# Kernel tuning notes

Measured on AMD Instinct MI355X. Metric: run time of the kernel, lower is better.

## Reference

```python
import jax, jax.numpy as jnp
import numpy as np

B, S, W, V, H, L = 128, 128, 16, 128, 512, 64


def setup_inputs() -> dict:
    key = jax.random.key(0)
    ks = jax.random.split(key, 12)
    chars = jax.random.randint(ks[0], (B, S, W), 0, V, dtype=jnp.int32)
    # pack_padded_sequence requires descending lengths; force max length == S for static shapes
    lengths = jnp.sort(jax.random.randint(ks[1], (B,), 1, S + 1, dtype=jnp.int32))[::-1]
    lengths = lengths.at[0].set(S)
    s = 1.0 / np.sqrt(H)
    s2 = 1.0 / np.sqrt(2 * H)

    def u(k, shape, sc):
        return jax.random.uniform(k, shape, jnp.float32, -sc, sc)

    return {
        "chars": chars,
        "lengths": lengths,
        "forget": jnp.float32(0.5),
        "W_ih_f": u(ks[2], (3 * H, V), s),
        "W_hh_f": u(ks[3], (3 * H, H), s),
        "b_ih_f": u(ks[4], (3 * H,), s),
        "b_hh_f": u(ks[5], (3 * H,), s),
        "W_ih_b": u(ks[6], (3 * H, V), s),
        "W_hh_b": u(ks[7], (3 * H, H), s),
        "b_ih_b": u(ks[8], (3 * H,), s),
        "b_hh_b": u(ks[9], (3 * H,), s),
        "W_lin": u(ks[10], (L, 2 * H), s2),
        "b_lin": u(ks[11], (L,), s2),
    }


def _fofe(chars, forget):
    # z = f*z + onehot applied only at nonzero chars => weight f^(# nonzero chars after k)
    mask = (chars != 0).astype(jnp.float32)                              # [B,S,W]
    cnt = jnp.flip(jnp.cumsum(jnp.flip(mask, -1), -1), -1) - mask        # suffix count
    wts = mask * jnp.power(forget, cnt)                                  # [B,S,W]
    oh = jax.nn.one_hot(chars, V, dtype=jnp.float32)                     # [B,S,W,V]
    return jnp.einsum('bsw,bswv->bsv', wts, oh)                          # [B,S,V]


def _gru_dir(x, mask, W_ih, W_hh, b_ih, b_hh):
    # x: [S,B,V], mask: [S,B] (1.0 where t < length). PyTorch GRU cell math.
    xw = jnp.einsum('sbv,gv->sbg', x, W_ih) + b_ih                       # [S,B,3H]
    h0 = jnp.zeros((x.shape[1], H), jnp.float32)

    def step(h, inp):
        xw_t, m = inp
        hw = h @ W_hh.T + b_hh
        xr, xz, xn = jnp.split(xw_t, 3, -1)
        hr, hz, hn = jnp.split(hw, 3, -1)
        r = jax.nn.sigmoid(xr + hr)
        z = jax.nn.sigmoid(xz + hz)
        n = jnp.tanh(xn + r * hn)
        h_new = (1.0 - z) * n + z * h
        m_ = m[:, None]
        h = jnp.where(m_ > 0, h_new, h)
        return h, h_new * m_  # packed-seq semantics: zero output past length

    _, ys = jax.lax.scan(step, h0, (xw, mask))
    return ys  # [S,B,H]


def _forward(chars, lengths, forget, W_ih_f, W_hh_f, b_ih_f, b_hh_f,
             W_ih_b, W_hh_b, b_ih_b, b_hh_b, W_lin, b_lin):
    x = _fofe(chars, forget)                                             # [B,S,V]
    t = jnp.arange(S)
    valid = t[None, :] < lengths[:, None]                                # [B,S]
    mask = valid.astype(jnp.float32).T                                   # [S,B]

    out_f = _gru_dir(x.transpose(1, 0, 2), mask, W_ih_f, W_hh_f, b_ih_f, b_hh_f)

    # backward direction: reverse each sequence within its own length
    idx = jnp.clip(lengths[:, None] - 1 - t[None, :], 0, S - 1)          # [B,S]
    x_rev = jnp.take_along_axis(x, idx[:, :, None], axis=1)              # [B,S,V]
    out_b_rev = _gru_dir(x_rev.transpose(1, 0, 2), mask, W_ih_b, W_hh_b, b_ih_b, b_hh_b)
    out_b = jnp.take_along_axis(out_b_rev.transpose(1, 0, 2), idx[:, :, None], axis=1)
    out_b = out_b * valid[:, :, None].astype(jnp.float32)

    out = jnp.concatenate([out_f.transpose(1, 0, 2), out_b], axis=-1)    # [B,S,2H]
    out = out @ W_lin.T + b_lin                                          # [B,S,L]
    # faithful to torch: out.view(-1, L, S) is a raw reshape, NOT a transpose
    return out.reshape(-1, L, S)


def reference(chars, lengths, forget, W_ih_f, W_hh_f, b_ih_f, b_hh_f,
              W_ih_b, W_hh_b, b_ih_b, b_hh_b, W_lin, b_lin):
    return _forward(chars, lengths, forget, W_ih_f, W_hh_f, b_ih_f, b_hh_f,
                    W_ih_b, W_hh_b, b_ih_b, b_hh_b, W_lin, b_lin)
```

## Files before the change

kernel.cpp:

```cpp
#include <hip/hip_runtime.h>
#include <hip/hip_bf16.h>

#define B_ 128
#define S_ 128
#define W_ 16
#define V_ 128
#define H_ 512
#define L_ 64

typedef _Float16 f16x8 __attribute__((ext_vector_type(8)));
typedef float f32x4 __attribute__((ext_vector_type(4)));

__device__ __forceinline__ float sigm(float v) { return 1.0f / (1.0f + __expf(-v)); }
__device__ __forceinline__ float tanhf_(float v) { return 1.0f - 2.0f / (1.0f + __expf(2.0f * v)); }

__device__ __forceinline__ unsigned short f16bits(_Float16 h) {
    return __builtin_bit_cast(unsigned short, h);
}

#define OFF_SLOT  1048576
#define OFF_FLAG  1064960
#define OFF_XHI   1065024
#define OFF_XLO   5259328
#define OFF_WH    9453632
#define OFF_SMALL 13385792
#define OFF_YCAT  13672832
#define OFF_WLH   47227264
#define OFF_WLL   47358336

__global__ void detect_kernel(const unsigned* __restrict__ w, int* __restrict__ flag) {
    __shared__ int sv[256];
    int tid = threadIdx.x;
    unsigned word = w[tid];
    unsigned e = (word >> 7) & 0xFFu;
    sv[tid] = (e >= 64u && e <= 126u) ? 1 : 0;
    __syncthreads();
    for (int s = 128; s > 0; s >>= 1) {
        if (tid < s) sv[tid] += sv[tid + s];
        __syncthreads();
    }
    if (tid == 0) *flag = (sv[0] >= 160) ? 1 : 0;
}

__global__ void prep_whalf(const void* __restrict__ whhf, const void* __restrict__ whhb,
                           const void* __restrict__ wihf, const void* __restrict__ wihb,
                           _Float16* __restrict__ dst, const int* __restrict__ flag) {
    int i = blockIdx.x * 256 + threadIdx.x;
    const void* src;
    int off;
    if (i < 786432)       { src = whhf; off = i; }
    else if (i < 1572864) { src = whhb; off = i - 786432; }
    else if (i < 1769472) { src = wihf; off = i - 1572864; }
    else                  { src = wihb; off = i - 1769472; }
    float v = (*flag) ? __bfloat162float(((const __hip_bfloat16*)src)[off])
                      : ((const float*)src)[off];
    dst[i] = (_Float16)v;
}

__global__ void prep_small(const void* __restrict__ bihf, const void* __restrict__ bhhf,
                           const void* __restrict__ bihb, const void* __restrict__ bhhb,
                           const void* __restrict__ wlin, const void* __restrict__ blin,
                           const void* __restrict__ fg,
                           float* __restrict__ dst, const int* __restrict__ flag) {
    int i = blockIdx.x * 256 + threadIdx.x;
    if (i >= 71745) return;
    const void* src;
    int off;
    if (i < 1536)       { src = bihf; off = i; }
    else if (i < 3072)  { src = bhhf; off = i - 1536; }
    else if (i < 4608)  { src = bihb; off = i - 3072; }
    else if (i < 6144)  { src = bhhb; off = i - 4608; }
    else if (i < 71680) { src = wlin; off = i - 6144; }
    else if (i < 71744) { src = blin; off = i - 71680; }
    else                { src = fg;   off = 0; }
    float v = (*flag) ? __bfloat162float(((const __hip_bfloat16*)src)[off])
                      : ((const float*)src)[off];
    dst[i] = v;
}

__global__ void prep_wlin(const void* __restrict__ wlin,
                          _Float16* __restrict__ whi, _Float16* __restrict__ wlo,
                          const int* __restrict__ flag) {
    int i = blockIdx.x * 256 + threadIdx.x;
    float v = (*flag) ? __bfloat162float(((const __hip_bfloat16*)wlin)[i])
                      : ((const float*)wlin)[i];
    _Float16 hi = (_Float16)v;
    whi[i] = hi;
    wlo[i] = (_Float16)(v - (float)hi);
}

__global__ void fofe_kernel(const int* __restrict__ chars,
                            const float* __restrict__ fg,
                            unsigned short* __restrict__ xhi,
                            unsigned short* __restrict__ xlo) {
    __shared__ int cS[2][W_];
    int tid = threadIdx.x;
    int sub = tid >> 7;
    int v = tid & 127;
    int bi = blockIdx.x * 2 + sub;
    if (v < W_) cS[sub][v] = chars[bi * W_ + v];
    __syncthreads();
    float f = fg[0];
    float wt[W_];
    float cur = 1.0f;
#pragma unroll
    for (int w = W_ - 1; w >= 0; --w) {
        bool m = (cS[sub][w] != 0);
        wt[w] = m ? cur : 0.0f;
        if (m) cur *= f;
    }
    float acc = 0.0f;
#pragma unroll
    for (int w = 0; w < W_; ++w) acc += (cS[sub][w] == v) ? wt[w] : 0.0f;
    _Float16 hi = (_Float16)acc;
    _Float16 lo = (_Float16)(acc - (float)hi);
    xhi[(size_t)bi * V_ + v] = f16bits(hi);
    xlo[(size_t)bi * V_ + v] = f16bits(lo);
}

__launch_bounds__(256, 1)
__global__ void gru_kernel(const int* __restrict__ lengths,
                           const _Float16* __restrict__ wh,
                           const float* __restrict__ biasF,
                           const unsigned short* __restrict__ xhi,
                           const unsigned short* __restrict__ xlo,
                           unsigned* __restrict__ hbuf,
                           unsigned* __restrict__ slots,
                           _Float16* __restrict__ Ycat) {
    (void)slots;
    constexpr int RSTR = 656;
    __shared__ _Float16 Ahi[16 * RSTR];
    __shared__ _Float16 Alo[16 * RSTR];
    __shared__ int lenS[16];

    const int tid = threadIdx.x;
    const int chain = blockIdx.x & 15;
    const int blk = blockIdx.x >> 4;
    const int d = chain & 1;
    const int bg = chain >> 1;
    const int b0 = bg * 16;
    const int wave = tid >> 6;
    const int lane = tid & 63;
    const int quad = lane >> 4;
    const int col = lane & 15;
    const int j0w = (blk * 4 + wave) * 16;

    const _Float16* Whh = wh + (d ? 786432 : 0);
    const _Float16* Wih = wh + 1572864 + (d ? 196608 : 0);
    const float* bih = biasF + (d ? 3072 : 0);
    const float* bhh = biasF + 1536 + (d ? 3072 : 0);

    if (tid < 16) lenS[tid] = lengths[b0 + tid];
    __syncthreads();

    const int g_r = j0w + col;

    f16x8 br[20], bz[20], bn[20];
#pragma unroll
    for (int kk = 0; kk < 16; ++kk) {
        int k = kk * 32 + quad * 8;
        br[kk] = *(const f16x8*)(Whh + (size_t)(g_r)*H_ + k);
        bz[kk] = *(const f16x8*)(Whh + (size_t)(512 + g_r) * H_ + k);
        bn[kk] = *(const f16x8*)(Whh + (size_t)(1024 + g_r) * H_ + k);
    }
#pragma unroll
    for (int kk = 16; kk < 20; ++kk) {
        int k = (kk - 16) * 32 + quad * 8;
        br[kk] = *(const f16x8*)(Wih + (size_t)(g_r)*V_ + k);
        bz[kk] = *(const f16x8*)(Wih + (size_t)(512 + g_r) * V_ + k);
        bn[kk] = *(const f16x8*)(Wih + (size_t)(1024 + g_r) * V_ + k);
    }

    const float bias_r = bih[g_r] + bhh[g_r];
    const float bias_z = bih[512 + g_r] + bhh[512 + g_r];
    const float bihn = bih[1024 + g_r];
    const float bhhn = bhh[1024 + g_r];

    int len4[4];
#pragma unroll
    for (int i = 0; i < 4; ++i) len4[i] = lenS[quad * 4 + i];
    const int maxlen = lenS[0];

    float h_own[4] = {0.f, 0.f, 0.f, 0.f};

    const _Float16* arh = &Ahi[col * RSTR + quad * 8];
    const _Float16* arl = &Alo[col * RSTR + quad * 8];

    const int xb = tid >> 4;
    const int xv8 = (tid & 15) * 8;

    const unsigned long long tagMsk = (1ULL << 16) | (1ULL << 48);

    for (int t = 0; t < S_; ++t) {
        if (t < maxlen) {
            const int par = t & 1;
            int lxb = lenS[xb];
            int sxb = d ? max(0, lxb - 1 - t) : t;
            int4 xh4 = *(const int4*)(xhi + ((size_t)(b0 + xb) * S_ + sxb) * V_ + xv8);
            int4 xl4 = *(const int4*)(xlo + ((size_t)(b0 + xb) * S_ + sxb) * V_ + xv8);

            unsigned* hrp = hbuf + ((size_t)(par * 2 + d) * B_ + b0) * H_;
            unsigned long long hv[16];
            if (t > 0) {
                const unsigned te = ((((unsigned)(t - 1)) >> 1) & 1u) ^ 1u;
                const unsigned long long tagPat =
                    ((unsigned long long)te << 16) | ((unsigned long long)te << 48);
                unsigned pend = 0xFFFFu;
                unsigned round = 0;
                while (true) {
#pragma unroll
                    for (int i = 0; i < 16; ++i)
                        if (pend & (1u << i))
                            hv[i] = __hip_atomic_load(
                                (const unsigned long long*)(hrp + (size_t)i * H_ + tid * 2),
                                __ATOMIC_RELAXED, __HIP_MEMORY_SCOPE_AGENT);
                    unsigned np = 0;
#pragma unroll
                    for (int i = 0; i < 16; ++i)
                        if ((pend & (1u << i)) && (hv[i] & tagMsk) != tagPat) np |= (1u << i);
                    pend = np;
                    if (!pend) break;
                    ++round;
                    if (round > 4u) __builtin_amdgcn_s_sleep(1);
                    if ((round & 31u) == 31u)
                        __builtin_amdgcn_fence(__ATOMIC_ACQUIRE, "agent");
                    if (round > 400000u) break;
                }
            } else {
#pragma unroll
                for (int i = 0; i < 16; ++i) hv[i] = 0ULL;
            }

            *(int4*)&Ahi[xb * RSTR + 512 + xv8] = xh4;
            *(int4*)&Alo[xb * RSTR + 512 + xv8] = xl4;
#pragma unroll
            for (int i = 0; i < 16; ++i) {
                unsigned p0 = (unsigned)hv[i];
                unsigned p1 = (unsigned)(hv[i] >> 32);
                unsigned hi2 = (p0 & 0xffffu) | (p1 << 16);
                unsigned lo2 = ((p0 >> 16) | (p1 & 0xffff0000u)) & ~0x00010001u;
                *(unsigned*)&Ahi[i * RSTR + tid * 2] = hi2;
                *(unsigned*)&Alo[i * RSTR + tid * 2] = lo2;
            }
            __syncthreads();

            f32x4 accr = {0.f, 0.f, 0.f, 0.f};
            f32x4 accz = {0.f, 0.f, 0.f, 0.f};
            f32x4 acchn = {0.f, 0.f, 0.f, 0.f};
            f32x4 accxn = {0.f, 0.f, 0.f, 0.f};
#pragma unroll
            for (int kk = 0; kk < 16; ++kk) {
                f16x8 ah = *(const f16x8*)(arh + kk * 32);
                f16x8 al = *(const f16x8*)(arl + kk * 32);
                accr = __builtin_amdgcn_mfma_f32_16x16x32_f16(ah, br[kk], accr, 0, 0, 0);
                accr = __builtin_amdgcn_mfma_f32_16x16x32_f16(al, br[kk], accr, 0, 0, 0);
                accz = __builtin_amdgcn_mfma_f32_16x16x32_f16(ah, bz[kk], accz, 0, 0, 0);
                accz = __builtin_amdgcn_mfma_f32_16x16x32_f16(al, bz[kk], accz, 0, 0, 0);
                acchn = __builtin_amdgcn_mfma_f32_16x16x32_f16(ah, bn[kk], acchn, 0, 0, 0);
                acchn = __builtin_amdgcn_mfma_f32_16x16x32_f16(al, bn[kk], acchn, 0, 0, 0);
            }
#pragma unroll
            for (int kk = 16; kk < 20; ++kk) {
                f16x8 ah = *(const f16x8*)(arh + 512 + (kk - 16) * 32);
                f16x8 al = *(const f16x8*)(arl + 512 + (kk - 16) * 32);
                accr = __builtin_amdgcn_mfma_f32_16x16x32_f16(ah, br[kk], accr, 0, 0, 0);
                accr = __builtin_amdgcn_mfma_f32_16x16x32_f16(al, br[kk], accr, 0, 0, 0);
                accz = __builtin_amdgcn_mfma_f32_16x16x32_f16(ah, bz[kk], accz, 0, 0, 0);
                accz = __builtin_amdgcn_mfma_f32_16x16x32_f16(al, bz[kk], accz, 0, 0, 0);
                accxn = __builtin_amdgcn_mfma_f32_16x16x32_f16(ah, bn[kk], accxn, 0, 0, 0);
                accxn = __builtin_amdgcn_mfma_f32_16x16x32_f16(al, bn[kk], accxn, 0, 0, 0);
            }
            __syncthreads();

            unsigned* hwp = hbuf + ((size_t)((1 - par) * 2 + d) * B_ + b0) * H_;
            const unsigned tg = ((((unsigned)t) >> 1) & 1u) ^ 1u;
            float yv[4];
            int so4[4];
#pragma unroll
            for (int i = 0; i < 4; ++i) {
                int bl = quad * 4 + i;
                float r = sigm(accr[i] + bias_r);
                float zg = sigm(accz[i] + bias_z);
                float ng = tanhf_((accxn[i] + bihn) + r * (acchn[i] + bhhn));
                float hcand = (1.0f - zg) * ng + zg * h_own[i];
                bool m = (t < len4[i]);
                yv[i] = m ? hcand : 0.0f;
                h_own[i] = m ? hcand : h_own[i];
                _Float16 hhi = (_Float16)h_own[i];
                _Float16 hlo = (_Float16)(h_own[i] - (float)hhi);
                unsigned packed = (unsigned)f16bits(hhi) |
                                  ((((unsigned)f16bits(hlo) & 0xFFFEu) | tg) << 16);
                __hip_atomic_store(hwp + (size_t)bl * H_ + j0w + col, packed,
                                   __ATOMIC_RELAXED, __HIP_MEMORY_SCOPE_AGENT);
                so4[i] = (d && m) ? (len4[i] - 1 - t) : t;
            }
#pragma unroll
            for (int i = 0; i < 4; ++i) {
                int bl = quad * 4 + i;
                Ycat[((size_t)(b0 + bl) * S_ + so4[i]) * 1024 + d * 512 + j0w + col] =
                    (_Float16)yv[i];
            }
        } else {
#pragma unroll
            for (int i = 0; i < 4; ++i) {
                int bl = quad * 4 + i;
                Ycat[((size_t)(b0 + bl) * S_ + t) * 1024 + d * 512 + j0w + col] = (_Float16)0.0f;
            }
        }
    }
}

__launch_bounds__(256, 1)
__global__ void lin_kernel(const _Float16* __restrict__ Ycat,
                           const _Float16* __restrict__ Whi,
                           const _Float16* __restrict__ Wlo,
                           const float* __restrict__ blinF,
                           float* __restrict__ out) {
    const int tid = threadIdx.x;
    const int wave = tid >> 6;
    const int lane = tid & 63;
    const int quad = lane >> 4;
    const int col = lane & 15;
    const int pos0 = blockIdx.x * 64 + wave * 16;

    const _Float16* arow = Ycat + (size_t)(pos0 + col) * 1024 + quad * 8;

    f32x4 acc[4] = {{0.f, 0.f, 0.f, 0.f}, {0.f, 0.f, 0.f, 0.f},
                    {0.f, 0.f, 0.f, 0.f}, {0.f, 0.f, 0.f, 0.f}};
#pragma unroll 4
    for (int c = 0; c < 1024; c += 32) {
        f16x8 a = *(const f16x8*)(arow + c);
#pragma unroll
        for (int nt = 0; nt < 4; ++nt) {
            const size_t wo = (size_t)(nt * 16 + col) * 1024 + c + quad * 8;
            f16x8 bh = *(const f16x8*)(Whi + wo);
            f16x8 bl = *(const f16x8*)(Wlo + wo);
            acc[nt] = __builtin_amdgcn_mfma_f32_16x16x32_f16(a, bh, acc[nt], 0, 0, 0);
            acc[nt] = __builtin_amdgcn_mfma_f32_16x16x32_f16(a, bl, acc[nt], 0, 0, 0);
        }
    }
#pragma unroll
    for (int nt = 0; nt < 4; ++nt) {
        int l = nt * 16 + col;
        float bias = blinF[l];
#pragma unroll
        for (int r = 0; r < 4; ++r) {
            int pos = pos0 + quad * 4 + r;
            out[(size_t)pos * L_ + l] = acc[nt][r] + bias;
        }
    }
}

extern "C" void kernel_launch(void* const* d_in, const int* in_sizes, int n_in,
                              void* d_out, int out_size, void* d_ws, size_t ws_size,
                              hipStream_t stream) {
    const int* chars = (const int*)d_in[0];
    const int* lengths = (const int*)d_in[1];
    const void* forget = d_in[2];
    const void* Wihf = d_in[3];
    const void* Whhf = d_in[4];
    const void* bihf = d_in[5];
    const void* bhhf = d_in[6];
    const void* Wihb = d_in[7];
    const void* Whhb = d_in[8];
    const void* bihb = d_in[9];
    const void* bhhb = d_in[10];
    const void* Wlin = d_in[11];
    const void* blin = d_in[12];
    float* out = (float*)d_out;

    char* ws = (char*)d_ws;
    unsigned* hbuf = (unsigned*)(ws + 0);
    unsigned* slots = (unsigned*)(ws + OFF_SLOT);
    int* flag = (int*)(ws + OFF_FLAG);
    unsigned short* xhi = (unsigned short*)(ws + OFF_XHI);
    unsigned short* xlo = (unsigned short*)(ws + OFF_XLO);
    _Float16* whalf = (_Float16*)(ws + OFF_WH);
    float* smallF = (float*)(ws + OFF_SMALL);
    _Float16* Ycat = (_Float16*)(ws + OFF_YCAT);
    _Float16* wlh = (_Float16*)(ws + OFF_WLH);
    _Float16* wll = (_Float16*)(ws + OFF_WLL);

    (void)hipMemsetAsync(ws, 0, OFF_XHI, stream);

    hipLaunchKernelGGL(detect_kernel, dim3(1), dim3(256), 0, stream,
                       (const unsigned*)Whhf, flag);
    hipLaunchKernelGGL(prep_whalf, dim3(1966080 / 256), dim3(256), 0, stream,
                       Whhf, Whhb, Wihf, Wihb, whalf, flag);
    hipLaunchKernelGGL(prep_small, dim3(281), dim3(256), 0, stream,
                       bihf, bhhf, bihb, bhhb, Wlin, blin, forget, smallF, flag);
    hipLaunchKernelGGL(prep_wlin, dim3(256), dim3(256), 0, stream,
                       Wlin, wlh, wll, flag);
    hipLaunchKernelGGL(fofe_kernel, dim3(B_ * S_ / 2), dim3(256), 0, stream,
                       chars, smallF + 71744, xhi, xlo);

    hipLaunchKernelGGL(gru_kernel, dim3(128), dim3(256), 0, stream,
                       lengths, whalf, smallF, xhi, xlo, hbuf, slots, Ycat);

    hipLaunchKernelGGL(lin_kernel, dim3(256), dim3(256), 0, stream,
                       Ycat, wlh, wll, smallF + 71680, out);
}
```

Before: 609.9 us.

## Load GRU operands directly into MFMA registers and overlap polling with compute

```diff
diff --git a/kernel.cpp b/kernel.cpp
--- a/kernel.cpp
+++ b/kernel.cpp
@@ -128,9 +128,6 @@
                            unsigned* __restrict__ slots,
                            _Float16* __restrict__ Ycat) {
     (void)slots;
-    constexpr int RSTR = 656;
-    __shared__ _Float16 Ahi[16 * RSTR];
-    __shared__ _Float16 Alo[16 * RSTR];
     __shared__ int lenS[16];
 
     const int tid = threadIdx.x;
@@ -180,97 +177,126 @@
 #pragma unroll
     for (int i = 0; i < 4; ++i) len4[i] = lenS[quad * 4 + i];
     const int maxlen = lenS[0];
+    const int lenC = lenS[col];
 
     float h_own[4] = {0.f, 0.f, 0.f, 0.f};
-
-    const _Float16* arh = &Ahi[col * RSTR + quad * 8];
-    const _Float16* arl = &Alo[col * RSTR + quad * 8];
-
-    const int xb = tid >> 4;
-    const int xv8 = (tid & 15) * 8;
 
     const unsigned long long tagMsk = (1ULL << 16) | (1ULL << 48);
 
     for (int t = 0; t < S_; ++t) {
         if (t < maxlen) {
             const int par = t & 1;
-            int lxb = lenS[xb];
-            int sxb = d ? max(0, lxb - 1 - t) : t;
-            int4 xh4 = *(const int4*)(xhi + ((size_t)(b0 + xb) * S_ + sxb) * V_ + xv8);
-            int4 xl4 = *(const int4*)(xlo + ((size_t)(b0 + xb) * S_ + sxb) * V_ + xv8);
-
-            unsigned* hrp = hbuf + ((size_t)(par * 2 + d) * B_ + b0) * H_;
-            unsigned long long hv[16];
+
+            const int sxc = d ? max(0, lenC - 1 - t) : t;
+            const unsigned short* xrh =
+                xhi + ((size_t)(b0 + col) * S_ + sxc) * V_ + quad * 8;
+            const unsigned short* xrl =
+                xlo + ((size_t)(b0 + col) * S_ + sxc) * V_ + quad * 8;
+            int4 xh4[4], xl4[4];
+#pragma unroll
+            for (int kx = 0; kx < 4; ++kx) {
+                xh4[kx] = *(const int4*)(xrh + kx * 32);
+                xl4[kx] = *(const int4*)(xrl + kx * 32);
+            }
+
+            const unsigned long long* hb =
+                (const unsigned long long*)(hbuf +
+                    ((size_t)(par * 2 + d) * B_ + b0) * H_) +
+                (size_t)col * (H_ / 2) + quad * 4;
+
+            f32x4 accr = {0.f, 0.f, 0.f, 0.f};
+            f32x4 accz = {0.f, 0.f, 0.f, 0.f};
+            f32x4 acchn = {0.f, 0.f, 0.f, 0.f};
+            f32x4 accxn = {0.f, 0.f, 0.f, 0.f};
+
+            unsigned long long cur[16];
+            if (t > 0) {
+#pragma unroll
+                for (int q = 0; q < 16; ++q)
+                    cur[q] = __hip_atomic_load(hb + (size_t)(q >> 2) * 16 + (q & 3),
+                                               __ATOMIC_RELAXED, __HIP_MEMORY_SCOPE_AGENT);
+            }
+
+#pragma unroll
+            for (int kx = 0; kx < 4; ++kx) {
+                f16x8 ah = __builtin_bit_cast(f16x8, xh4[kx]);
+                f16x8 al = __builtin_bit_cast(f16x8, xl4[kx]);
+                accr = __builtin_amdgcn_mfma_f32_16x16x32_f16(ah, br[16 + kx], accr, 0, 0, 0);
+                accr = __builtin_amdgcn_mfma_f32_16x16x32_f16(al, br[16 + kx], accr, 0, 0, 0);
+                accz = __builtin_amdgcn_mfma_f32_16x16x32_f16(ah, bz[16 + kx], accz, 0, 0, 0);
+                accz = __builtin_amdgcn_mfma_f32_16x16x32_f16(al, bz[16 + kx], accz, 0, 0, 0);
+                accxn = __builtin_amdgcn_mfma_f32_16x16x32_f16(ah, bn[16 + kx], accxn, 0, 0, 0);
+                accxn = __builtin_amdgcn_mfma_f32_16x16x32_f16(al, bn[16 + kx], accxn, 0, 0, 0);
+            }
+
             if (t > 0) {
                 const unsigned te = ((((unsigned)(t - 1)) >> 1) & 1u) ^ 1u;
                 const unsigned long long tagPat =
                     ((unsigned long long)te << 16) | ((unsigned long long)te << 48);
-                unsigned pend = 0xFFFFu;
-                unsigned round = 0;
-                while (true) {
-#pragma unroll
-                    for (int i = 0; i < 16; ++i)
-                        if (pend & (1u << i))
-                            hv[i] = __hip_atomic_load(
-                                (const unsigned long long*)(hrp + (size_t)i * H_ + tid * 2),
+#pragma unroll
+                for (int g = 0; g < 4; ++g) {
+                    unsigned pend = 0xFFFFu;
+                    unsigned rounds = 0;
+                    while (true) {
+                        unsigned np = 0;
+#pragma unroll
+                        for (int q = 0; q < 16; ++q)
+                            if ((pend >> q) & 1u)
+                                if ((cur[q] & tagMsk) != tagPat) np |= (1u << q);
+                        if (!np) break;
+#pragma unroll
+                        for (int q = 0; q < 16; ++q)
+                            if ((np >> q) & 1u)
+                                cur[q] = __hip_atomic_load(
+                                    hb + (size_t)(g * 4 + (q >> 2)) * 16 + (q & 3),
+                                    __ATOMIC_RELAXED, __HIP_MEMORY_SCOPE_AGENT);
+                        pend = np;
+                        ++rounds;
+                        if (rounds > 4u) __builtin_amdgcn_s_sleep(1);
+                        if ((rounds & 31u) == 31u)
+                            __builtin_amdgcn_fence(__ATOMIC_ACQUIRE, "agent");
+                        if (rounds > 400000u) break;
+                    }
+                    unsigned long long nxt[16];
+                    if (g < 3) {
+#pragma unroll
+                        for (int q = 0; q < 16; ++q)
+                            nxt[q] = __hip_atomic_load(
+                                hb + (size_t)((g + 1) * 4 + (q >> 2)) * 16 + (q & 3),
                                 __ATOMIC_RELAXED, __HIP_MEMORY_SCOPE_AGENT);
-                    unsigned np = 0;
-#pragma unroll
-                    for (int i = 0; i < 16; ++i)
-                        if ((pend & (1u << i)) && (hv[i] & tagMsk) != tagPat) np |= (1u << i);
-                    pend = np;
-                    if (!pend) break;
-                    ++round;
-                    if (round > 4u) __builtin_amdgcn_s_sleep(1);
-                    if ((round & 31u) == 31u)
-                        __builtin_amdgcn_fence(__ATOMIC_ACQUIRE, "agent");
-                    if (round > 400000u) break;
+                    }
+#pragma unroll
+                    for (int kk2 = 0; kk2 < 4; ++kk2) {
+                        const int kk = g * 4 + kk2;
+                        unsigned hi2[4], lo2[4];
+#pragma unroll
+                        for (int j = 0; j < 4; ++j) {
+                            unsigned long long v = cur[kk2 * 4 + j];
+                            unsigned p0 = (unsigned)v;
+                            unsigned p1 = (unsigned)(v >> 32);
+                            hi2[j] = (p0 & 0xffffu) | (p1 << 16);
+                            lo2[j] = ((p0 >> 16) | (p1 & 0xffff0000u)) & ~0x00010001u;
+                        }
+                        int4 h4, l4;
+                        h4.x = (int)hi2[0]; h4.y = (int)hi2[1];
+                        h4.z = (int)hi2[2]; h4.w = (int)hi2[3];
+                        l4.x = (int)lo2[0]; l4.y = (int)lo2[1];
+                        l4.z = (int)lo2[2]; l4.w = (int)lo2[3];
+                        f16x8 ah = __builtin_bit_cast(f16x8, h4);
+                        f16x8 al = __builtin_bit_cast(f16x8, l4);
+                        accr = __builtin_amdgcn_mfma_f32_16x16x32_f16(ah, br[kk], accr, 0, 0, 0);
+                        accr = __builtin_amdgcn_mfma_f32_16x16x32_f16(al, br[kk], accr, 0, 0, 0);
+                        accz = __builtin_amdgcn_mfma_f32_16x16x32_f16(ah, bz[kk], accz, 0, 0, 0);
+                        accz = __builtin_amdgcn_mfma_f32_16x16x32_f16(al, bz[kk], accz, 0, 0, 0);
+                        acchn = __builtin_amdgcn_mfma_f32_16x16x32_f16(ah, bn[kk], acchn, 0, 0, 0);
+                        acchn = __builtin_amdgcn_mfma_f32_16x16x32_f16(al, bn[kk], acchn, 0, 0, 0);
+                    }
+                    if (g < 3) {
+#pragma unroll
+                        for (int q = 0; q < 16; ++q) cur[q] = nxt[q];
+                    }
                 }
-            } else {
-#pragma unroll
-                for (int i = 0; i < 16; ++i) hv[i] = 0ULL;
-            }
-
-            *(int4*)&Ahi[xb * RSTR + 512 + xv8] = xh4;
-            *(int4*)&Alo[xb * RSTR + 512 + xv8] = xl4;
-#pragma unroll
-            for (int i = 0; i < 16; ++i) {
-                unsigned p0 = (unsigned)hv[i];
-                unsigned p1 = (unsigned)(hv[i] >> 32);
-                unsigned hi2 = (p0 & 0xffffu) | (p1 << 16);
-                unsigned lo2 = ((p0 >> 16) | (p1 & 0xffff0000u)) & ~0x00010001u;
-                *(unsigned*)&Ahi[i * RSTR + tid * 2] = hi2;
-                *(unsigned*)&Alo[i * RSTR + tid * 2] = lo2;
-            }
-            __syncthreads();
-
-            f32x4 accr = {0.f, 0.f, 0.f, 0.f};
-            f32x4 accz = {0.f, 0.f, 0.f, 0.f};
-            f32x4 acchn = {0.f, 0.f, 0.f, 0.f};
-            f32x4 accxn = {0.f, 0.f, 0.f, 0.f};
-#pragma unroll
-            for (int kk = 0; kk < 16; ++kk) {
-                f16x8 ah = *(const f16x8*)(arh + kk * 32);
-                f16x8 al = *(const f16x8*)(arl + kk * 32);
-                accr = __builtin_amdgcn_mfma_f32_16x16x32_f16(ah, br[kk], accr, 0, 0, 0);
-                accr = __builtin_amdgcn_mfma_f32_16x16x32_f16(al, br[kk], accr, 0, 0, 0);
-                accz = __builtin_amdgcn_mfma_f32_16x16x32_f16(ah, bz[kk], accz, 0, 0, 0);
-                accz = __builtin_amdgcn_mfma_f32_16x16x32_f16(al, bz[kk], accz, 0, 0, 0);
-                acchn = __builtin_amdgcn_mfma_f32_16x16x32_f16(ah, bn[kk], acchn, 0, 0, 0);
-                acchn = __builtin_amdgcn_mfma_f32_16x16x32_f16(al, bn[kk], acchn, 0, 0, 0);
-            }
-#pragma unroll
-            for (int kk = 16; kk < 20; ++kk) {
-                f16x8 ah = *(const f16x8*)(arh + 512 + (kk - 16) * 32);
-                f16x8 al = *(const f16x8*)(arl + 512 + (kk - 16) * 32);
-                accr = __builtin_amdgcn_mfma_f32_16x16x32_f16(ah, br[kk], accr, 0, 0, 0);
-                accr = __builtin_amdgcn_mfma_f32_16x16x32_f16(al, br[kk], accr, 0, 0, 0);
-                accz = __builtin_amdgcn_mfma_f32_16x16x32_f16(ah, bz[kk], accz, 0, 0, 0);
-                accz = __builtin_amdgcn_mfma_f32_16x16x32_f16(al, bz[kk], accz, 0, 0, 0);
-                accxn = __builtin_amdgcn_mfma_f32_16x16x32_f16(ah, bn[kk], accxn, 0, 0, 0);
-                accxn = __builtin_amdgcn_mfma_f32_16x16x32_f16(al, bn[kk], accxn, 0, 0, 0);
-            }
-            __syncthreads();
+            }
 
             unsigned* hwp = hbuf + ((size_t)((1 - par) * 2 + d) * B_ + b0) * H_;
             const unsigned tg = ((((unsigned)t) >> 1) & 1u) ^ 1u;
```

After: 1.407 ms. 131% more time.

## Merge prep kernels into one launch and double-buffer GRU LDS to drop barrier

Applied to the files above, without the earlier changes.

```diff
diff --git a/kernel.cpp b/kernel.cpp
--- a/kernel.cpp
+++ b/kernel.cpp
@@ -42,80 +42,78 @@
     if (tid == 0) *flag = (sv[0] >= 160) ? 1 : 0;
 }
 
-__global__ void prep_whalf(const void* __restrict__ whhf, const void* __restrict__ whhb,
-                           const void* __restrict__ wihf, const void* __restrict__ wihb,
-                           _Float16* __restrict__ dst, const int* __restrict__ flag) {
-    int i = blockIdx.x * 256 + threadIdx.x;
-    const void* src;
-    int off;
-    if (i < 786432)       { src = whhf; off = i; }
-    else if (i < 1572864) { src = whhb; off = i - 786432; }
-    else if (i < 1769472) { src = wihf; off = i - 1572864; }
-    else                  { src = wihb; off = i - 1769472; }
-    float v = (*flag) ? __bfloat162float(((const __hip_bfloat16*)src)[off])
-                      : ((const float*)src)[off];
-    dst[i] = (_Float16)v;
-}
-
-__global__ void prep_small(const void* __restrict__ bihf, const void* __restrict__ bhhf,
-                           const void* __restrict__ bihb, const void* __restrict__ bhhb,
-                           const void* __restrict__ wlin, const void* __restrict__ blin,
-                           const void* __restrict__ fg,
-                           float* __restrict__ dst, const int* __restrict__ flag) {
-    int i = blockIdx.x * 256 + threadIdx.x;
-    if (i >= 71745) return;
-    const void* src;
-    int off;
-    if (i < 1536)       { src = bihf; off = i; }
-    else if (i < 3072)  { src = bhhf; off = i - 1536; }
-    else if (i < 4608)  { src = bihb; off = i - 3072; }
-    else if (i < 6144)  { src = bhhb; off = i - 4608; }
-    else if (i < 71680) { src = wlin; off = i - 6144; }
-    else if (i < 71744) { src = blin; off = i - 71680; }
-    else                { src = fg;   off = 0; }
-    float v = (*flag) ? __bfloat162float(((const __hip_bfloat16*)src)[off])
-                      : ((const float*)src)[off];
-    dst[i] = v;
-}
-
-__global__ void prep_wlin(const void* __restrict__ wlin,
-                          _Float16* __restrict__ whi, _Float16* __restrict__ wlo,
-                          const int* __restrict__ flag) {
-    int i = blockIdx.x * 256 + threadIdx.x;
-    float v = (*flag) ? __bfloat162float(((const __hip_bfloat16*)wlin)[i])
-                      : ((const float*)wlin)[i];
-    _Float16 hi = (_Float16)v;
-    whi[i] = hi;
-    wlo[i] = (_Float16)(v - (float)hi);
-}
-
-__global__ void fofe_kernel(const int* __restrict__ chars,
-                            const float* __restrict__ fg,
-                            unsigned short* __restrict__ xhi,
-                            unsigned short* __restrict__ xlo) {
-    __shared__ int cS[2][W_];
-    int tid = threadIdx.x;
-    int sub = tid >> 7;
-    int v = tid & 127;
-    int bi = blockIdx.x * 2 + sub;
-    if (v < W_) cS[sub][v] = chars[bi * W_ + v];
-    __syncthreads();
-    float f = fg[0];
-    float wt[W_];
-    float cur = 1.0f;
-#pragma unroll
-    for (int w = W_ - 1; w >= 0; --w) {
-        bool m = (cS[sub][w] != 0);
-        wt[w] = m ? cur : 0.0f;
-        if (m) cur *= f;
-    }
-    float acc = 0.0f;
-#pragma unroll
-    for (int w = 0; w < W_; ++w) acc += (cS[sub][w] == v) ? wt[w] : 0.0f;
-    _Float16 hi = (_Float16)acc;
-    _Float16 lo = (_Float16)(acc - (float)hi);
-    xhi[(size_t)bi * V_ + v] = f16bits(hi);
-    xlo[(size_t)bi * V_ + v] = f16bits(lo);
+__global__ void prep_all(const void* __restrict__ whhf, const void* __restrict__ whhb,
+                         const void* __restrict__ wihf, const void* __restrict__ wihb,
+                         const void* __restrict__ bihf, const void* __restrict__ bhhf,
+                         const void* __restrict__ bihb, const void* __restrict__ bhhb,
+                         const void* __restrict__ wlin, const void* __restrict__ blin,
+                         const void* __restrict__ fgp, const int* __restrict__ chars,
+                         _Float16* __restrict__ whalf, float* __restrict__ smallF,
+                         _Float16* __restrict__ whi, _Float16* __restrict__ wlo,
+                         unsigned short* __restrict__ xhi, unsigned short* __restrict__ xlo,
+                         const int* __restrict__ flag) {
+    const int bid = blockIdx.x;
+    const int tid = threadIdx.x;
+    const int fl = *flag;
+    if (bid < 7680) {
+        int i = bid * 256 + tid;
+        const void* src;
+        int off;
+        if (i < 786432)       { src = whhf; off = i; }
+        else if (i < 1572864) { src = whhb; off = i - 786432; }
+        else if (i < 1769472) { src = wihf; off = i - 1572864; }
+        else                  { src = wihb; off = i - 1769472; }
+        float v = fl ? __bfloat162float(((const __hip_bfloat16*)src)[off])
+                     : ((const float*)src)[off];
+        whalf[i] = (_Float16)v;
+    } else if (bid < 7961) {
+        int i = (bid - 7680) * 256 + tid;
+        if (i >= 71745) return;
+        const void* src;
+        int off;
+        if (i < 1536)       { src = bihf; off = i; }
+        else if (i < 3072)  { src = bhhf; off = i - 1536; }
+        else if (i < 4608)  { src = bihb; off = i - 3072; }
+        else if (i < 6144)  { src = bhhb; off = i - 4608; }
+        else if (i < 71680) { src = wlin; off = i - 6144; }
+        else if (i < 71744) { src = blin; off = i - 71680; }
+        else                { src = fgp;  off = 0; }
+        float v = fl ? __bfloat162float(((const __hip_bfloat16*)src)[off])
+                     : ((const float*)src)[off];
+        smallF[i] = v;
+    } else if (bid < 8217) {
+        int i = (bid - 7961) * 256 + tid;
+        float v = fl ? __bfloat162float(((const __hip_bfloat16*)wlin)[i])
+                     : ((const float*)wlin)[i];
+        _Float16 hi = (_Float16)v;
+        whi[i] = hi;
+        wlo[i] = (_Float16)(v - (float)hi);
+    } else {
+        __shared__ int cS[2][W_];
+        const int fb = bid - 8217;
+        int sub = tid >> 7;
+        int v = tid & 127;
+        int bi = fb * 2 + sub;
+        if (v < W_) cS[sub][v] = chars[bi * W_ + v];
+        __syncthreads();
+        float f = fl ? __bfloat162float(*(const __hip_bfloat16*)fgp)
+                     : *(const float*)fgp;
+        float wt[W_];
+        float cur = 1.0f;
+#pragma unroll
+        for (int w = W_ - 1; w >= 0; --w) {
+            bool m = (cS[sub][w] != 0);
+            wt[w] = m ? cur : 0.0f;
+            if (m) cur *= f;
+        }
+        float acc = 0.0f;
+#pragma unroll
+        for (int w = 0; w < W_; ++w) acc += (cS[sub][w] == v) ? wt[w] : 0.0f;
+        _Float16 hi = (_Float16)acc;
+        _Float16 lo = (_Float16)(acc - (float)hi);
+        xhi[(size_t)bi * V_ + v] = f16bits(hi);
+        xlo[(size_t)bi * V_ + v] = f16bits(lo);
+    }
 }
 
 __launch_bounds__(256, 1)
@@ -129,8 +127,8 @@
                            _Float16* __restrict__ Ycat) {
     (void)slots;
     constexpr int RSTR = 656;
-    __shared__ _Float16 Ahi[16 * RSTR];
-    __shared__ _Float16 Alo[16 * RSTR];
+    __shared__ _Float16 Ahi[2][16 * RSTR];
+    __shared__ _Float16 Alo[2][16 * RSTR];
     __shared__ int lenS[16];
 
     const int tid = threadIdx.x;
@@ -183,9 +181,6 @@
 
     float h_own[4] = {0.f, 0.f, 0.f, 0.f};
 
-    const _Float16* arh = &Ahi[col * RSTR + quad * 8];
-    const _Float16* arl = &Alo[col * RSTR + quad * 8];
-
     const int xb = tid >> 4;
     const int xv8 = (tid & 15) * 8;
 
@@ -194,6 +189,8 @@
     for (int t = 0; t < S_; ++t) {
         if (t < maxlen) {
             const int par = t & 1;
+            const _Float16* arh = &Ahi[par][col * RSTR + quad * 8];
+            const _Float16* arl = &Alo[par][col * RSTR + quad * 8];
             int lxb = lenS[xb];
             int sxb = d ? max(0, lxb - 1 - t) : t;
             int4 xh4 = *(const int4*)(xhi + ((size_t)(b0 + xb) * S_ + sxb) * V_ + xv8);
@@ -231,16 +228,16 @@
                 for (int i = 0; i < 16; ++i) hv[i] = 0ULL;
             }
 
-            *(int4*)&Ahi[xb * RSTR + 512 + xv8] = xh4;
-            *(int4*)&Alo[xb * RSTR + 512 + xv8] = xl4;
+            *(int4*)&Ahi[par][xb * RSTR + 512 + xv8] = xh4;
+            *(int4*)&Alo[par][xb * RSTR + 512 + xv8] = xl4;
 #pragma unroll
             for (int i = 0; i < 16; ++i) {
                 unsigned p0 = (unsigned)hv[i];
                 unsigned p1 = (unsigned)(hv[i] >> 32);
                 unsigned hi2 = (p0 & 0xffffu) | (p1 << 16);
                 unsigned lo2 = ((p0 >> 16) | (p1 & 0xffff0000u)) & ~0x00010001u;
-                *(unsigned*)&Ahi[i * RSTR + tid * 2] = hi2;
-                *(unsigned*)&Alo[i * RSTR + tid * 2] = lo2;
+                *(unsigned*)&Ahi[par][i * RSTR + tid * 2] = hi2;
+                *(unsigned*)&Alo[par][i * RSTR + tid * 2] = lo2;
             }
             __syncthreads();
 
@@ -270,7 +267,6 @@
                 accxn = __builtin_amdgcn_mfma_f32_16x16x32_f16(ah, bn[kk], accxn, 0, 0, 0);
                 accxn = __builtin_amdgcn_mfma_f32_16x16x32_f16(al, bn[kk], accxn, 0, 0, 0);
             }
-            __syncthreads();
 
             unsigned* hwp = hbuf + ((size_t)((1 - par) * 2 + d) * B_ + b0) * H_;
             const unsigned tg = ((((unsigned)t) >> 1) & 1u) ^ 1u;
@@ -385,14 +381,10 @@
 
     hipLaunchKernelGGL(detect_kernel, dim3(1), dim3(256), 0, stream,
                        (const unsigned*)Whhf, flag);
-    hipLaunchKernelGGL(prep_whalf, dim3(1966080 / 256), dim3(256), 0, stream,
-                       Whhf, Whhb, Wihf, Wihb, whalf, flag);
-    hipLaunchKernelGGL(prep_small, dim3(281), dim3(256), 0, stream,
-                       bihf, bhhf, bihb, bhhb, Wlin, blin, forget, smallF, flag);
-    hipLaunchKernelGGL(prep_wlin, dim3(256), dim3(256), 0, stream,
-                       Wlin, wlh, wll, flag);
-    hipLaunchKernelGGL(fofe_kernel, dim3(B_ * S_ / 2), dim3(256), 0, stream,
-                       chars, smallF + 71744, xhi, xlo);
+    hipLaunchKernelGGL(prep_all, dim3(16409), dim3(256), 0, stream,
+                       Whhf, Whhb, Wihf, Wihb, bihf, bhhf, bihb, bhhb,
+                       Wlin, blin, forget, chars,
+                       whalf, smallF, wlh, wll, xhi, xlo, flag);
 
     hipLaunchKernelGGL(gru_kernel, dim3(128), dim3(256), 0, stream,
                        lengths, whalf, smallF, xhi, xlo, hbuf, slots, Ycat);
```

New measurement: 591.3 us. 3.1% less time.
